# Optimization experiments

Hardware: AMD Instinct MI355X
Metric: run time of the kernel (lower is better)

The kernel has to match this reference:

```python
import jax, jax.numpy as jnp
import numpy as np


def setup_inputs() -> dict:
    key = jax.random.key(0)
    k1, k2, k3 = jax.random.split(key, 3)
    B, N, D = 16, 512, 256
    # integer frame durations per token, 4..11 frames (avg ~7.5)
    durations = jax.random.randint(k1, (B, N), 4, 12, dtype=jnp.int32)
    # T = max over batch of total frames (static python int, mirrors torch.arange(0, max(s)))
    total_len = int(jnp.max(jnp.sum(durations, axis=-1)))
    x = jax.random.normal(k2, (B, N, D), dtype=jnp.float32)
    # positive Gaussian range (std) per token
    ranges = jax.random.uniform(k3, (B, N), minval=0.5, maxval=4.0, dtype=jnp.float32)
    return {"x": x, "durations": durations, "ranges": ranges, "total_len": total_len}


def _gaussian_weights(durations, ranges, total_len):
    # e: cumulative end frame per token, c: Gaussian center per token
    e = jnp.cumsum(durations, axis=-1).astype(jnp.float32)          # [B, N]
    c = (e - 0.5 * durations.astype(jnp.float32))[..., None]        # [B, N, 1]
    t = jnp.arange(total_len, dtype=jnp.float32)[None, None, :]     # [1, 1, T]
    inv_r2 = ranges[..., None] ** (-2)                               # [B, N, 1]
    w1 = jnp.exp(-inv_r2 * (t - c) ** 2)                             # [B, N, T]
    # original computes the exp twice (w_1 and inside w_2); same math, computed once
    w2 = jnp.sum(w1, axis=1, keepdims=True) + 1e-20                  # [B, 1, T]
    return w1 / w2


def _create_positions(durations, total_len):
    # frame-index-within-token positions: pos[b, t] = t - start_of_segment(t)
    e = jnp.cumsum(durations, axis=-1)                               # [B, N]
    starts = e - durations                                           # [B, N]
    t = jnp.arange(total_len, dtype=durations.dtype)                 # [T]
    seg = jax.vmap(lambda eb: jnp.searchsorted(eb, t, side='right'))(e)  # [B, T]
    seg = jnp.clip(seg, 0, durations.shape[-1] - 1)
    return t[None, :] - jnp.take_along_axis(starts, seg, axis=-1)    # [B, T]


def reference(x, durations, ranges, total_len):
    weights = _gaussian_weights(durations, ranges, total_len)        # [B, N, T]
    # matmul(weights.transpose(1,2), x) -> [B, T, D]
    out = jnp.einsum('bnt,bnd->btd', weights, x)
    positions = _create_positions(durations, total_len)
    return positions, out, weights
```

## Files before the change

### kernel.cpp

```cpp
#include <hip/hip_runtime.h>
#include <hip/hip_bf16.h>


#define NWC 44
#define TT  64
#define MARGIN 42.0f

__global__ void scan_kernel(const int* __restrict__ dur,
                            const float* __restrict__ ranges,
                            float* __restrict__ c, float* __restrict__ ir,
                            int* __restrict__ e_i, int* __restrict__ st_i) {
    const int N = 512;
    int b = blockIdx.x, tid = threadIdx.x;
    __shared__ int sc[512];
    int d = dur[b * N + tid];
    sc[tid] = d;
    __syncthreads();
    for (int off = 1; off < 512; off <<= 1) {
        int add = (tid >= off) ? sc[tid - off] : 0;
        __syncthreads();
        sc[tid] += add;
        __syncthreads();
    }
    int e = sc[tid];
    float r = ranges[b * N + tid];
    c[b * N + tid]   = (float)e - 0.5f * (float)d;
    ir[b * N + tid]  = 1.0f / (r * r);
    e_i[b * N + tid] = e;
    st_i[b * N + tid] = e - d;
}

__global__ void pos_kernel(const int* __restrict__ e_i, const int* __restrict__ st_i,
                           float* __restrict__ pos_out, int T) {
    const int N = 512;
    int b = blockIdx.y;
    int t = blockIdx.x * 256 + threadIdx.x;
    __shared__ int es[512], ss[512];
    for (int i = threadIdx.x; i < 512; i += 256) {
        es[i] = e_i[b * N + i];
        ss[i] = st_i[b * N + i];
    }
    __syncthreads();
    if (t >= T) return;
    int lo = 0, hi = 512;
    while (lo < hi) {
        int m = (lo + hi) >> 1;
        if (es[m] <= t) lo = m + 1; else hi = m;
    }
    int seg = min(lo, 511);
    pos_out[b * T + t] = (float)(t - ss[seg]);
}

__global__ __launch_bounds__(256) void wout_kernel(
        const float* __restrict__ x, const float* __restrict__ c,
        const float* __restrict__ ir,
        float* __restrict__ out1 , float* __restrict__ out2 ,
        int T) {
    const int N = 512, D = 256;
    int b = blockIdx.y;
    int t0 = blockIdx.x * TT;
    int tid = threadIdx.x;

    __shared__ float c_s[512];
    __shared__ float ir_s[512];
    __shared__ __align__(16) float w_s[TT][NWC];
    __shared__ float part[4][TT];
    __shared__ float iw2_s[TT];
    __shared__ int lohi[2];

    for (int i = tid; i < 512; i += 256) {
        c_s[i]  = c[b * N + i];
        ir_s[i] = ir[b * N + i];
    }
    __syncthreads();

    if (tid == 0) {
        float lo_v = (float)t0 - MARGIN;
        float hi_v = (float)(t0 + TT - 1) + MARGIN;
        int lo = 0, hi = 512;
        while (lo < hi) { int m = (lo + hi) >> 1; if (c_s[m] < lo_v) lo = m + 1; else hi = m; }
        int l = lo;
        lo = 0; hi = 512;
        while (lo < hi) { int m = (lo + hi) >> 1; if (c_s[m] <= hi_v) lo = m + 1; else hi = m; }
        int h = lo - 1;
        if (h > l + NWC - 1) h = l + NWC - 1;
        lohi[0] = l; lohi[1] = h;
    }
    __syncthreads();
    int lo_u = lohi[0], hi_u = lohi[1];

    int tl = tid & 63;
    int s  = tid >> 6;
    int t  = t0 + tl;

    float p = 0.f;
    for (int i = s; i < NWC; i += 4) {
        int n = lo_u + i;
        float w1 = 0.f;
        if (n <= hi_u && t < T) {
            float d = (float)t - c_s[n];
            w1 = expf(-ir_s[n] * d * d);
        }
        w_s[tl][i] = w1;
        p += w1;
    }
    part[s][tl] = p;
    __syncthreads();
    if (tid < 64) {
        float w2 = part[0][tid] + part[1][tid] + part[2][tid] + part[3][tid];
        iw2_s[tid] = 1.0f / (w2 + 1e-20f);
    }
    __syncthreads();

    float xr[NWC];
    #pragma unroll
    for (int i = 0; i < NWC; i++) {
        int n = lo_u + i;
        xr[i] = (n <= hi_u) ? x[(b * N + n) * D + tid] : 0.f;
    }
    for (int tl2 = 0; tl2 < TT; tl2++) {
        int tt = t0 + tl2;
        if (tt >= T) break;
        const float4* wrow = (const float4*)&w_s[tl2][0];
        float acc = 0.f;
        #pragma unroll
        for (int q = 0; q < NWC / 4; q++) {
            float4 w4 = wrow[q];
            acc += w4.x * xr[4 * q + 0];
            acc += w4.y * xr[4 * q + 1];
            acc += w4.z * xr[4 * q + 2];
            acc += w4.w * xr[4 * q + 3];
        }
        out1[(b * T + tt) * D + tid] = acc * iw2_s[tl2];
    }

    if (t < T) {
        int wbase = b * N * T + t;
        float iw2 = iw2_s[tl];
        for (int j = 0; j < 512; j += 4) {
            int nn = j + s;
            int i = nn - lo_u;
            float v = 0.f;
            if (i >= 0 && nn <= hi_u) v = w_s[tl][i] * iw2;
            out2[wbase + nn * T] = v;
        }
    }
}

extern "C" void kernel_launch(void* const* d_in, const int* in_sizes, int n_in,
                              void* d_out, int out_size, void* d_ws, size_t ws_size,
                              hipStream_t stream) {
    const float* x      = (const float*)d_in[0];
    const int*   dur    = (const int*)d_in[1];
    const float* ranges = (const float*)d_in[2];
    const int B = 16, N = 512, D = 256;
    const int T = out_size / (B * (1 + D + N));

    float* pos_out = (float*)d_out;
    float* out1    = pos_out + (size_t)B * T;
    float* out2    = out1 + (size_t)B * T * D;

    float* c  = (float*)d_ws;
    float* ir = c + B * N;
    int*   e_i  = (int*)(ir + B * N);
    int*   st_i = e_i + B * N;

    scan_kernel<<<B, 512, 0, stream>>>(dur, ranges, c, ir, e_i, st_i);

    dim3 g2((T + 255) / 256, B);
    pos_kernel<<<g2, 256, 0, stream>>>(e_i, st_i, pos_out, T);

    dim3 g3((T + TT - 1) / TT, B);
    wout_kernel<<<g3, 256, 0, stream>>>(x, c, ir, out1, out2, T);
}
```

Before: 241.3 us.

## Use bf16 MFMA for weighted sum and fuse position kernel into main kernel

Replaces the per-thread scalar FMA loop over a 44-token window with 16x16x32 bf16 MFMA instructions. Weights are stored in a padded bf16 shared buffer of 64 tokens, and x is converted to bf16 on load. The positions computation is folded into the weight kernel, which removes one launch. The change also reshapes the weight loop and pads shared memory. bf16 inputs lower the precision of the output matmul, and the x loads are now strided gathers per token row.

Result: faster. 233.9 us (-3.0%).

```diff
diff --git a/kernel.cpp b/kernel.cpp
--- a/kernel.cpp
+++ b/kernel.cpp
@@ -2,9 +2,22 @@
 #include <hip/hip_bf16.h>
 
 
+#define TT  64
 #define NWC 44
-#define TT  64
+#define KP  64
+#define WSS 45
+#define WBS 72
 #define MARGIN 42.0f
+
+typedef __attribute__((ext_vector_type(8))) short short8;
+typedef __attribute__((ext_vector_type(8))) unsigned short ushort8;
+typedef __attribute__((ext_vector_type(4))) float f32x4;
+
+__device__ inline unsigned short f2bf(float f) {
+    union { float f; unsigned int u; } v; v.f = f;
+    unsigned int u = v.u;
+    return (unsigned short)((u + 0x7FFFu + ((u >> 16) & 1u)) >> 16);
+}
 
 __global__ void scan_kernel(const int* __restrict__ dur,
                             const float* __restrict__ ranges,
@@ -24,36 +37,17 @@
     }
     int e = sc[tid];
     float r = ranges[b * N + tid];
-    c[b * N + tid]   = (float)e - 0.5f * (float)d;
-    ir[b * N + tid]  = 1.0f / (r * r);
-    e_i[b * N + tid] = e;
+    c[b * N + tid]    = (float)e - 0.5f * (float)d;
+    ir[b * N + tid]   = 1.0f / (r * r);
+    e_i[b * N + tid]  = e;
     st_i[b * N + tid] = e - d;
-}
-
-__global__ void pos_kernel(const int* __restrict__ e_i, const int* __restrict__ st_i,
-                           float* __restrict__ pos_out, int T) {
-    const int N = 512;
-    int b = blockIdx.y;
-    int t = blockIdx.x * 256 + threadIdx.x;
-    __shared__ int es[512], ss[512];
-    for (int i = threadIdx.x; i < 512; i += 256) {
-        es[i] = e_i[b * N + i];
-        ss[i] = st_i[b * N + i];
-    }
-    __syncthreads();
-    if (t >= T) return;
-    int lo = 0, hi = 512;
-    while (lo < hi) {
-        int m = (lo + hi) >> 1;
-        if (es[m] <= t) lo = m + 1; else hi = m;
-    }
-    int seg = min(lo, 511);
-    pos_out[b * T + t] = (float)(t - ss[seg]);
 }
 
 __global__ __launch_bounds__(256) void wout_kernel(
         const float* __restrict__ x, const float* __restrict__ c,
         const float* __restrict__ ir,
+        const int* __restrict__ e_i, const int* __restrict__ st_i,
+        float* __restrict__ pos_out ,
         float* __restrict__ out1 , float* __restrict__ out2 ,
         int T) {
     const int N = 512, D = 256;
@@ -63,7 +57,9 @@
 
     __shared__ float c_s[512];
     __shared__ float ir_s[512];
-    __shared__ __align__(16) float w_s[TT][NWC];
+    __shared__ int   es[512], ss[512];
+    __shared__ float w_s[TT][WSS];
+    __shared__ __align__(16) unsigned short wb[TT][WBS];
     __shared__ float part[4][TT];
     __shared__ float iw2_s[TT];
     __shared__ int lohi[2];
@@ -71,6 +67,8 @@
     for (int i = tid; i < 512; i += 256) {
         c_s[i]  = c[b * N + i];
         ir_s[i] = ir[b * N + i];
+        es[i]   = e_i[b * N + i];
+        ss[i]   = st_i[b * N + i];
     }
     __syncthreads();
 
@@ -86,6 +84,15 @@
         if (h > l + NWC - 1) h = l + NWC - 1;
         lohi[0] = l; lohi[1] = h;
     }
+    if (tid < TT) {
+        int t = t0 + tid;
+        if (t < T) {
+            int lo = 0, hi = 512;
+            while (lo < hi) { int m = (lo + hi) >> 1; if (es[m] <= t) lo = m + 1; else hi = m; }
+            int seg = min(lo, 511);
+            pos_out[b * T + t] = (float)(t - ss[seg]);
+        }
+    }
     __syncthreads();
     int lo_u = lohi[0], hi_u = lohi[1];
 
@@ -94,55 +101,80 @@
     int t  = t0 + tl;
 
     float p = 0.f;
-    for (int i = s; i < NWC; i += 4) {
+    #pragma unroll
+    for (int jj = 0; jj < 16; jj++) {
+        int i = s + 4 * jj;
         int n = lo_u + i;
         float w1 = 0.f;
         if (n <= hi_u && t < T) {
             float d = (float)t - c_s[n];
-            w1 = expf(-ir_s[n] * d * d);
-        }
-        w_s[tl][i] = w1;
+            w1 = __expf(-ir_s[n] * d * d) == 0.f ? 0.f : expf(-ir_s[n] * d * d);
+        }
+        wb[tl][i] = f2bf(w1);
+        if (i < NWC) w_s[tl][i] = w1;
         p += w1;
     }
     part[s][tl] = p;
     __syncthreads();
-    if (tid < 64) {
+    if (tid < TT) {
         float w2 = part[0][tid] + part[1][tid] + part[2][tid] + part[3][tid];
         iw2_s[tid] = 1.0f / (w2 + 1e-20f);
     }
     __syncthreads();
 
-    float xr[NWC];
-    #pragma unroll
-    for (int i = 0; i < NWC; i++) {
-        int n = lo_u + i;
-        xr[i] = (n <= hi_u) ? x[(b * N + n) * D + tid] : 0.f;
-    }
-    for (int tl2 = 0; tl2 < TT; tl2++) {
-        int tt = t0 + tl2;
-        if (tt >= T) break;
-        const float4* wrow = (const float4*)&w_s[tl2][0];
-        float acc = 0.f;
+    int lane = tid & 63;
+    int l15  = lane & 15;
+    int q    = lane >> 4;
+
+    f32x4 acc[16];
+    #pragma unroll
+    for (int nt = 0; nt < 16; nt++) acc[nt] = (f32x4){0.f, 0.f, 0.f, 0.f};
+
+    const float* xb = x + (size_t)b * N * D;
+    #pragma unroll
+    for (int ks = 0; ks < 2; ks++) {
+        short8 afrag = *(const short8*)&wb[16 * s + l15][ks * 32 + q * 8];
+        const float* rp[8];
         #pragma unroll
-        for (int q = 0; q < NWC / 4; q++) {
-            float4 w4 = wrow[q];
-            acc += w4.x * xr[4 * q + 0];
-            acc += w4.y * xr[4 * q + 1];
-            acc += w4.z * xr[4 * q + 2];
-            acc += w4.w * xr[4 * q + 3];
-        }
-        out1[(b * T + tt) * D + tid] = acc * iw2_s[tl2];
+        for (int j = 0; j < 8; j++) {
+            int tok = lo_u + ks * 32 + q * 8 + j;
+            tok = min(tok, 511);
+            rp[j] = xb + (size_t)tok * D;
+        }
+        #pragma unroll
+        for (int nt = 0; nt < 16; nt++) {
+            int d = nt * 16 + l15;
+            ushort8 bu;
+            #pragma unroll
+            for (int j = 0; j < 8; j++) bu[j] = f2bf(rp[j][d]);
+            short8 bfrag = (short8)bu;
+            acc[nt] = __builtin_amdgcn_mfma_f32_16x16x32_bf16(afrag, bfrag, acc[nt], 0, 0, 0);
+        }
+    }
+
+    float iwq[4];
+    #pragma unroll
+    for (int r = 0; r < 4; r++) iwq[r] = iw2_s[16 * s + q * 4 + r];
+    #pragma unroll
+    for (int r = 0; r < 4; r++) {
+        int tt = t0 + 16 * s + q * 4 + r;
+        if (tt < T) {
+            float* orow = out1 + ((size_t)b * T + tt) * D;
+            #pragma unroll
+            for (int nt = 0; nt < 16; nt++)
+                orow[nt * 16 + l15] = acc[nt][r] * iwq[r];
+        }
     }
 
     if (t < T) {
-        int wbase = b * N * T + t;
+        size_t wbase = (size_t)b * N * T + t;
         float iw2 = iw2_s[tl];
         for (int j = 0; j < 512; j += 4) {
             int nn = j + s;
             int i = nn - lo_u;
             float v = 0.f;
             if (i >= 0 && nn <= hi_u) v = w_s[tl][i] * iw2;
-            out2[wbase + nn * T] = v;
+            out2[wbase + (size_t)nn * T] = v;
         }
     }
 }
@@ -160,16 +192,13 @@
     float* out1    = pos_out + (size_t)B * T;
     float* out2    = out1 + (size_t)B * T * D;
 
-    float* c  = (float*)d_ws;
-    float* ir = c + B * N;
+    float* c    = (float*)d_ws;
+    float* ir   = c + B * N;
     int*   e_i  = (int*)(ir + B * N);
     int*   st_i = e_i + B * N;
 
     scan_kernel<<<B, 512, 0, stream>>>(dur, ranges, c, ir, e_i, st_i);
 
-    dim3 g2((T + 255) / 256, B);
-    pos_kernel<<<g2, 256, 0, stream>>>(e_i, st_i, pos_out, T);
-
     dim3 g3((T + TT - 1) / TT, B);
-    wout_kernel<<<g3, 256, 0, stream>>>(x, c, ir, out1, out2, T);
-}
+    wout_kernel<<<g3, 256, 0, stream>>>(x, c, ir, e_i, st_i, pos_out, out1, out2, T);
+}
```
